# Performance work log

Hardware: AMD Instinct MI355X
Metric: run time of the kernel (lower is better)

Reference implementation:

```python
import jax, jax.numpy as jnp
import numpy as np

B, C, IMG, P = 32, 3, 224, 16
HID, L, NH, DH, INTER, NCLS = 768, 12, 12, 64, 3072, 1000
GP = IMG // P  # 14 patches per side
S = GP * GP + 1  # 197 tokens
EPS = 1e-5  # torch LayerNorm default


def layer_norm(x, scale, bias):
    mu = jnp.mean(x, axis=-1, keepdims=True)
    var = jnp.mean(jnp.square(x - mu), axis=-1, keepdims=True)
    return (x - mu) * jax.lax.rsqrt(var + EPS) * scale + bias


def setup_inputs() -> dict:
    key = jax.random.key(0)
    ks = jax.random.split(key, 16)
    s = 0.02
    d = {
        "x": jax.random.normal(ks[0], (B, C, IMG, IMG), jnp.float32),
        "conv_w": jax.random.normal(ks[1], (HID, C, P, P), jnp.float32) * s,
        "conv_b": jnp.zeros((HID,), jnp.float32),
        "cls_token": jax.random.normal(ks[2], (1, 1, HID), jnp.float32),
        "pos_emb": jax.random.normal(ks[3], (1, S, HID), jnp.float32) * s,
        "ln1_s": jnp.ones((L, HID), jnp.float32),
        "ln1_b": jnp.zeros((L, HID), jnp.float32),
        "wq": jax.random.normal(ks[4], (L, NH, HID, DH), jnp.float32) * s,
        "bq": jnp.zeros((L, NH, DH), jnp.float32),
        "wk": jax.random.normal(ks[5], (L, NH, HID, DH), jnp.float32) * s,
        "bk": jnp.zeros((L, NH, DH), jnp.float32),
        "wv": jax.random.normal(ks[6], (L, NH, HID, DH), jnp.float32) * s,
        "bv": jnp.zeros((L, NH, DH), jnp.float32),
        "wo": jax.random.normal(ks[7], (L, HID, HID), jnp.float32) * s,
        "bo": jnp.zeros((L, HID), jnp.float32),
        "ln2_s": jnp.ones((L, HID), jnp.float32),
        "ln2_b": jnp.zeros((L, HID), jnp.float32),
        "w1": jax.random.normal(ks[8], (L, HID, INTER), jnp.float32) * s,
        "b1": jnp.zeros((L, INTER), jnp.float32),
        "w2": jax.random.normal(ks[9], (L, INTER, HID), jnp.float32) * s,
        "b2": jnp.zeros((L, HID), jnp.float32),
        "head_w": jax.random.normal(ks[10], (HID, NCLS), jnp.float32) * s,
        "head_b": jnp.zeros((NCLS,), jnp.float32),
    }
    return d


def vit_forward(x, conv_w, conv_b, cls_token, pos_emb, ln1_s, ln1_b,
                wq, bq, wk, bk, wv, bv, wo, bo, ln2_s, ln2_b,
                w1, b1, w2, b2, head_w, head_b):
    # Patch embedding: conv stride=kernel=P  ==  patch extract + matmul
    xp = x.reshape(B, C, GP, P, GP, P)
    h = jnp.einsum('bcipjq,dcpq->bijd', xp, conv_w) + conv_b  # [B,GP,GP,HID]
    h = h.reshape(B, GP * GP, HID)
    h = jnp.concatenate([jnp.broadcast_to(cls_token, (B, 1, HID)), h], axis=1)
    h = h + pos_emb  # [B,S,HID]

    scale = 1.0 / np.sqrt(DH).astype(np.float32)
    for l in range(L):
        # --- multi-head attention (per-head linears expressed as stacked einsum) ---
        hn = layer_norm(h, ln1_s[l], ln1_b[l])
        q = jnp.einsum('bsd,hdk->bhsk', hn, wq[l]) + bq[l][None, :, None, :]
        k = jnp.einsum('bsd,hdk->bhsk', hn, wk[l]) + bk[l][None, :, None, :]
        v = jnp.einsum('bsd,hdk->bhsk', hn, wv[l]) + bv[l][None, :, None, :]
        scores = jnp.einsum('bhsk,bhtk->bhst', q, k) * scale
        probs = jax.nn.softmax(scores, axis=-1)
        att = jnp.einsum('bhst,bhtk->bhsk', probs, v)  # [B,NH,S,DH]
        att = att.transpose(0, 2, 1, 3).reshape(B, S, HID)  # concat heads on last dim
        h = h + att @ wo[l] + bo[l]
        # --- MLP ---
        hn = layer_norm(h, ln2_s[l], ln2_b[l])
        m = jax.nn.gelu(hn @ w1[l] + b1[l], approximate=False)
        h = h + m @ w2[l] + b2[l]

    # classifier on [CLS] token
    return h[:, 0, :] @ head_w + head_b  # [B, NCLS]


def reference(x, conv_w, conv_b, cls_token, pos_emb, ln1_s, ln1_b,
              wq, bq, wk, bk, wv, bv, wo, bo, ln2_s, ln2_b,
              w1, b1, w2, b2, head_w, head_b):
    return vit_forward(x, conv_w, conv_b, cls_token, pos_emb, ln1_s, ln1_b,
                       wq, bq, wk, bk, wv, bv, wo, bo, ln2_s, ln2_b,
                       w1, b1, w2, b2, head_w, head_b)
```

## Files before the change

### kernel.cpp

```cpp
#include <hip/hip_runtime.h>
#include <hip/hip_bf16.h>
#include <math.h>


using bf16 = __hip_bfloat16;
typedef __attribute__((ext_vector_type(8))) short short8;
typedef __attribute__((ext_vector_type(4))) float floatx4;

__device__ __forceinline__ void async_copy16(const bf16* g, bf16* l) {
    __builtin_amdgcn_global_load_lds(
        (const __attribute__((address_space(1))) void*)g,
        (__attribute__((address_space(3))) void*)l, 16, 0, 0);
}

__device__ __forceinline__ void wave_sync_vm0() {
    asm volatile("s_waitcnt vmcnt(0)" ::: "memory");
    __builtin_amdgcn_s_barrier();
    asm volatile("" ::: "memory");
}

template<int OUT_BF16, int ACT_GELU, int RESID>
__global__ __launch_bounds__(512, 4) void gemm_nt(
    const bf16* __restrict__ A, const bf16* __restrict__ B, void* __restrict__ Cout,
    const float* __restrict__ resid, const float* __restrict__ bias, float scale,
    int M, int N, int K, int lda, int ldb, int ldc,
    int batchInner, long sAi, long sAo, long sBi, long sBo, long sCi, long sCo)
{
    __shared__ __align__(16) bf16 As[2][128 * 32];
    __shared__ __align__(16) bf16 Bs[2][128 * 32];

    const int bz = blockIdx.z;
    const int bi = bz % batchInner, bo = bz / batchInner;
    const bf16* Ab = A + (long)bi * sAi + (long)bo * sAo;
    const bf16* Bb = B + (long)bi * sBi + (long)bo * sBo;
    const long coff = (long)bi * sCi + (long)bo * sCo;

    const int nbx = gridDim.x;
    const int nwg = nbx * gridDim.y;
    const int orig = blockIdx.y * nbx + blockIdx.x;
    const int q8 = nwg >> 3, r8 = nwg & 7;
    const int xcd = orig & 7, sidx = orig >> 3;
    const int wg = (xcd < r8 ? xcd * (q8 + 1) : r8 * (q8 + 1) + (xcd - r8) * q8) + sidx;
    const int m0 = (wg / nbx) << 7;
    const int n0 = (wg % nbx) << 7;

    const int tid  = threadIdx.x;
    const int lane = tid & 63;
    const int wave = tid >> 6;
    const int wrow = (wave >> 1) << 5;
    const int wcol = (wave & 1) << 6;
    const int quad = lane >> 4;
    const int l16  = lane & 15;

    floatx4 acc[2][4];
#pragma unroll
    for (int i = 0; i < 2; i++)
#pragma unroll
        for (int j = 0; j < 4; j++) acc[i][j] = (floatx4)0.0f;

    const int rIn = lane >> 2;
    const int seg = (lane & 3) << 3;
    const int rA = wave * 16 + rIn;
    const long aOff = (long)min(m0 + rA, M - 1) * lda + seg;
    const long bOff = (long)min(n0 + rA, N - 1) * ldb + seg;

    auto stage = [&](int buf, int kt) {
        const long kb = (long)kt << 5;
        async_copy16(Ab + aOff + kb, &As[buf][wave * 512]);
        async_copy16(Bb + bOff + kb, &Bs[buf][wave * 512]);
    };

    auto compute = [&](const bf16* __restrict__ Asb, const bf16* __restrict__ Bsb) {
        short8 af[2], bfr[4];
#pragma unroll
        for (int i = 0; i < 2; i++)
            af[i]  = *(const short8*)(&Asb[(wrow + i * 16 + l16) * 32 + quad * 8]);
#pragma unroll
        for (int j = 0; j < 4; j++)
            bfr[j] = *(const short8*)(&Bsb[(wcol + j * 16 + l16) * 32 + quad * 8]);
#pragma unroll
        for (int i = 0; i < 2; i++)
#pragma unroll
            for (int j = 0; j < 4; j++)
                acc[i][j] = __builtin_amdgcn_mfma_f32_16x16x32_bf16(
                    af[i], bfr[j], acc[i][j], 0, 0, 0);
    };

    const int kTiles = K >> 5;
    stage(0, 0);
    for (int kt = 0; kt < kTiles; kt += 2) {
        wave_sync_vm0();
        if (kt + 1 < kTiles) stage(1, kt + 1);
        compute(As[0], Bs[0]);
        if (kt + 1 < kTiles) {
            wave_sync_vm0();
            if (kt + 2 < kTiles) stage(0, kt + 2);
            compute(As[1], Bs[1]);
        }
    }

#pragma unroll
    for (int i = 0; i < 2; i++) {
        const int rbase = m0 + wrow + i * 16 + quad * 4;
#pragma unroll
        for (int j = 0; j < 4; j++) {
            const int col = n0 + wcol + j * 16 + l16;
            if (col >= N) continue;
            const float bval = bias ? bias[col] : 0.0f;
#pragma unroll
            for (int r = 0; r < 4; r++) {
                const int row = rbase + r;
                if (row >= M) continue;
                const long idx = coff + (long)row * ldc + col;
                float v = acc[i][j][r] * scale + bval;
                if (RESID)    v += resid[idx];
                if (ACT_GELU) v = 0.5f * v * (1.0f + erff(v * 0.70710678118654752f));
                if (OUT_BF16) ((bf16*)Cout)[idx] = __float2bfloat16(v);
                else          ((float*)Cout)[idx] = v;
            }
        }
    }
}

__global__ __launch_bounds__(256) void transpose_cvt(
    const float* __restrict__ src, bf16* __restrict__ dst, int K, int N,
    int srcLd, int dstLd, int batchInner, long sSi, long sSo, long sDi, long sDo)
{
    __shared__ float t[32][33];
    const int bz = blockIdx.z;
    const int bi = bz % batchInner, bo = bz / batchInner;
    const float* S = src + (long)bi * sSi + (long)bo * sSo;
    bf16* D = dst + (long)bi * sDi + (long)bo * sDo;
    const int k0 = blockIdx.y << 5, n0 = blockIdx.x << 5;
    const int tx = threadIdx.x & 31, ty = threadIdx.x >> 5;
#pragma unroll
    for (int i = 0; i < 32; i += 8) {
        int k = k0 + ty + i, n = n0 + tx;
        if (k < K && n < N) t[ty + i][tx] = S[(long)k * srcLd + n];
    }
    __syncthreads();
#pragma unroll
    for (int i = 0; i < 32; i += 8) {
        int n = n0 + ty + i, k = k0 + tx;
        if (n < N && k < K) D[(long)n * dstLd + k] = __float2bfloat16(t[tx][ty + i]);
    }
}

__global__ void cvt_f2b(const float* __restrict__ s, bf16* __restrict__ d, int n) {
    int i = blockIdx.x * 256 + threadIdx.x;
    if (i < n) d[i] = __float2bfloat16(s[i]);
}

__global__ void pack_qkv_bias(const float* __restrict__ bq, const float* __restrict__ bk,
                              const float* __restrict__ bv, float* __restrict__ qb) {
    int i = blockIdx.x * 256 + threadIdx.x;
    int l = i / 2304, n = i % 2304;
    float v = (n < 768) ? bq[l * 768 + n]
            : (n < 1536) ? bk[l * 768 + n - 768]
                         : bv[l * 768 + n - 1536];
    qb[i] = v;
}

__global__ __launch_bounds__(256) void im2col_k(const float* __restrict__ x, bf16* __restrict__ out) {
    const int row = blockIdx.x;
    const int b = row / 196, r = row % 196, gi = r / 14, gj = r % 14;
    const float* xb = x + (long)b * 3 * 224 * 224;
    bf16* o = out + (long)row * 768;
    const int tid = threadIdx.x;
#pragma unroll
    for (int i = 0; i < 3; i++) {
        int col = tid + (i << 8);
        int c = col >> 8, rem = col & 255, p = rem >> 4, q = rem & 15;
        o[col] = __float2bfloat16(xb[((long)c * 224 + gi * 16 + p) * 224 + gj * 16 + q]);
    }
}

__global__ __launch_bounds__(256) void assemble_k(const float* __restrict__ hp,
                                                  const float* __restrict__ cls,
                                                  const float* __restrict__ pos,
                                                  float* __restrict__ h) {
    const int row = blockIdx.x;
    const int b = row / 197, t = row % 197;
    float* o = h + (long)row * 768;
    const float* p = pos + (long)t * 768;
    const int tid = threadIdx.x;
#pragma unroll
    for (int i = 0; i < 3; i++) {
        int c = tid + (i << 8);
        float v = (t == 0) ? cls[c] : hp[((long)(b * 196 + t - 1)) * 768 + c];
        o[c] = v + p[c];
    }
}

__global__ __launch_bounds__(256) void layernorm_k(const float* __restrict__ h,
                                                   const float* __restrict__ gamma,
                                                   const float* __restrict__ beta,
                                                   bf16* __restrict__ out) {
    const int row = blockIdx.x;
    const float* x = h + (long)row * 768;
    const int tid = threadIdx.x;
    float v[3], s = 0.f, ss = 0.f;
#pragma unroll
    for (int i = 0; i < 3; i++) { v[i] = x[tid + (i << 8)]; s += v[i]; ss += v[i] * v[i]; }
#pragma unroll
    for (int o = 32; o; o >>= 1) { s += __shfl_xor(s, o); ss += __shfl_xor(ss, o); }
    __shared__ float red[8];
    const int wave = tid >> 6, lane = tid & 63;
    if (lane == 0) { red[wave] = s; red[4 + wave] = ss; }
    __syncthreads();
    if (tid == 0) {
        red[0] = red[0] + red[1] + red[2] + red[3];
        red[4] = red[4] + red[5] + red[6] + red[7];
    }
    __syncthreads();
    const float mu  = red[0] * (1.0f / 768.0f);
    const float var = red[4] * (1.0f / 768.0f) - mu * mu;
    const float inv = rsqrtf(var + 1e-5f);
    bf16* o = out + (long)row * 768;
#pragma unroll
    for (int i = 0; i < 3; i++) {
        int c = tid + (i << 8);
        o[c] = __float2bfloat16((v[i] - mu) * inv * gamma[c] + beta[c]);
    }
}

__global__ __launch_bounds__(256) void transpose_v(const bf16* __restrict__ qkv,
                                                   bf16* __restrict__ vT) {
    __shared__ bf16 t[64][65];
    const int t0 = blockIdx.x << 6;
    const int bz = blockIdx.y;
    const int b = bz / 12, hh = bz % 12;
    const int tx = threadIdx.x & 63, ty = threadIdx.x >> 6;
#pragma unroll
    for (int i = 0; i < 64; i += 4) {
        int tt = t0 + ty + i;
        bf16 v = __float2bfloat16(0.0f);
        if (tt < 197) v = qkv[((long)(b * 197 + tt)) * 2304 + 1536 + hh * 64 + tx];
        t[ty + i][tx] = v;
    }
    __syncthreads();
    bf16* d = vT + (long)bz * 14336;
#pragma unroll
    for (int i = 0; i < 64; i += 4) {
        int tt = t0 + tx;
        if (tt < 224) d[(long)(ty + i) * 224 + tt] = t[tx][ty + i];
    }
}

__global__ __launch_bounds__(256) void softmax_k(bf16* __restrict__ sc) {
    const int row = blockIdx.x * 4 + (threadIdx.x >> 6);
    const int lane = threadIdx.x & 63;
    bf16* s = sc + (long)row * 224;
    float v0 = __bfloat162float(s[lane]);
    float v1 = __bfloat162float(s[64 + lane]);
    float v2 = __bfloat162float(s[128 + lane]);
    float v3 = (192 + lane < 197) ? __bfloat162float(s[192 + lane]) : -1e30f;
    float m = fmaxf(fmaxf(v0, v1), fmaxf(v2, v3));
#pragma unroll
    for (int o = 32; o; o >>= 1) m = fmaxf(m, __shfl_xor(m, o));
    float e0 = __expf(v0 - m), e1 = __expf(v1 - m), e2 = __expf(v2 - m);
    float e3 = (192 + lane < 197) ? __expf(v3 - m) : 0.0f;
    float t = e0 + e1 + e2 + e3;
#pragma unroll
    for (int o = 32; o; o >>= 1) t += __shfl_xor(t, o);
    const float inv = 1.0f / t;
    s[lane]        = __float2bfloat16(e0 * inv);
    s[64 + lane]   = __float2bfloat16(e1 * inv);
    s[128 + lane]  = __float2bfloat16(e2 * inv);
    if (192 + lane < 224) s[192 + lane] = __float2bfloat16(e3 * inv);
}

__global__ __launch_bounds__(256) void extract_cls(const float* __restrict__ h,
                                                   bf16* __restrict__ hcls) {
    const int b = blockIdx.x, tid = threadIdx.x;
#pragma unroll
    for (int i = 0; i < 3; i++) {
        int c = tid + (i << 8);
        hcls[(long)b * 768 + c] = __float2bfloat16(h[(long)b * 197 * 768 + c]);
    }
}

extern "C" void kernel_launch(void* const* d_in, const int* in_sizes, int n_in,
                              void* d_out, int out_size, void* d_ws, size_t ws_size,
                              hipStream_t stream)
{
    (void)in_sizes; (void)n_in; (void)out_size; (void)ws_size;
    const float* x      = (const float*)d_in[0];
    const float* conv_w = (const float*)d_in[1];
    const float* conv_b = (const float*)d_in[2];
    const float* cls    = (const float*)d_in[3];
    const float* pos    = (const float*)d_in[4];
    const float* ln1_s  = (const float*)d_in[5];
    const float* ln1_b  = (const float*)d_in[6];
    const float* wq     = (const float*)d_in[7];
    const float* bq     = (const float*)d_in[8];
    const float* wk     = (const float*)d_in[9];
    const float* bk     = (const float*)d_in[10];
    const float* wv     = (const float*)d_in[11];
    const float* bv     = (const float*)d_in[12];
    const float* wo     = (const float*)d_in[13];
    const float* bo     = (const float*)d_in[14];
    const float* ln2_s  = (const float*)d_in[15];
    const float* ln2_b  = (const float*)d_in[16];
    const float* w1     = (const float*)d_in[17];
    const float* b1     = (const float*)d_in[18];
    const float* w2     = (const float*)d_in[19];
    const float* b2     = (const float*)d_in[20];
    const float* head_w = (const float*)d_in[21];
    const float* head_b = (const float*)d_in[22];
    float* out = (float*)d_out;

    char* ws = (char*)d_ws;
    size_t off = 0;
    auto take = [&](size_t bytes) -> char* {
        char* p = ws + off; off += (bytes + 255) & ~(size_t)255; return p;
    };
    float* h    = (float*)take(6304UL * 768 * 4);
    bf16*  hn   = (bf16*) take(6304UL * 768 * 2);
    bf16*  qkv  = (bf16*) take(6304UL * 2304 * 2);
    bf16*  att  = (bf16*) take(6304UL * 768 * 2);
    bf16*  Wqkv = (bf16*) take(12UL * 2304 * 768 * 2);
    bf16*  Wo   = (bf16*) take(12UL * 768 * 768 * 2);
    bf16*  W1   = (bf16*) take(12UL * 768 * 3072 * 2);
    bf16*  W2   = (bf16*) take(12UL * 768 * 3072 * 2);
    bf16*  Wp   = (bf16*) take(589824UL * 2);
    bf16*  Wh   = (bf16*) take(768000UL * 2);
    float* qb   = (float*)take(27648UL * 4);
    bf16*  hcls = (bf16*) take(24576UL * 2);
    char*  scr  = take(46UL * 1024 * 1024);
    bf16*  scores = (bf16*)scr;
    bf16*  vT     = (bf16*)(scr + 384UL * 197 * 224 * 2);
    bf16*  inter  = (bf16*)scr;
    bf16*  Apatch = (bf16*)scr;
    float* hpatch = (float*)(scr + ((6272UL * 768 * 2 + 255) & ~(size_t)255));

    cvt_f2b<<<2304, 256, 0, stream>>>(conv_w, Wp, 589824);
    transpose_cvt<<<dim3(2, 24, 144), 256, 0, stream>>>(wq, Wqkv,           768, 64, 64, 768, 12, 49152, 589824, 49152, 1769472);
    transpose_cvt<<<dim3(2, 24, 144), 256, 0, stream>>>(wk, Wqkv + 589824,  768, 64, 64, 768, 12, 49152, 589824, 49152, 1769472);
    transpose_cvt<<<dim3(2, 24, 144), 256, 0, stream>>>(wv, Wqkv + 1179648, 768, 64, 64, 768, 12, 49152, 589824, 49152, 1769472);
    transpose_cvt<<<dim3(24, 24, 12), 256, 0, stream>>>(wo, Wo, 768, 768, 768, 768, 12, 589824, 0, 589824, 0);
    transpose_cvt<<<dim3(96, 24, 12), 256, 0, stream>>>(w1, W1, 768, 3072, 3072, 768, 12, 2359296, 0, 2359296, 0);
    transpose_cvt<<<dim3(24, 96, 12), 256, 0, stream>>>(w2, W2, 3072, 768, 768, 3072, 12, 2359296, 0, 2359296, 0);
    transpose_cvt<<<dim3(32, 24, 1), 256, 0, stream>>>(head_w, Wh, 768, 1000, 1000, 768, 1, 0, 0, 0, 0);
    pack_qkv_bias<<<108, 256, 0, stream>>>(bq, bk, bv, qb);

    im2col_k<<<6272, 256, 0, stream>>>(x, Apatch);
    gemm_nt<0, 0, 0><<<dim3(6, 49, 1), 512, 0, stream>>>(
        Apatch, Wp, hpatch, nullptr, conv_b, 1.0f,
        6272, 768, 768, 768, 768, 768, 1, 0, 0, 0, 0, 0, 0);
    assemble_k<<<6304, 256, 0, stream>>>(hpatch, cls, pos, h);

    for (int l = 0; l < 12; ++l) {
        layernorm_k<<<6304, 256, 0, stream>>>(h, ln1_s + l * 768, ln1_b + l * 768, hn);
        gemm_nt<1, 0, 0><<<dim3(18, 50, 1), 512, 0, stream>>>(
            hn, Wqkv + (size_t)l * 1769472, qkv, nullptr, qb + l * 2304, 1.0f,
            6304, 2304, 768, 768, 768, 2304, 1, 0, 0, 0, 0, 0, 0);
        transpose_v<<<dim3(4, 384), 256, 0, stream>>>(qkv, vT);
        gemm_nt<1, 0, 0><<<dim3(2, 2, 384), 512, 0, stream>>>(
            qkv, qkv + 768, scores, nullptr, nullptr, 0.125f,
            197, 197, 64, 2304, 2304, 224,
            12, 64, 197L * 2304, 64, 197L * 2304, 44128, 529536);
        softmax_k<<<18912, 256, 0, stream>>>(scores);
        gemm_nt<1, 0, 0><<<dim3(1, 2, 384), 512, 0, stream>>>(
            scores, vT, att, nullptr, nullptr, 1.0f,
            197, 64, 224, 224, 224, 768,
            12, 44128, 529536, 14336, 172032, 64, 151296);
        gemm_nt<0, 0, 1><<<dim3(6, 50, 1), 512, 0, stream>>>(
            att, Wo + (size_t)l * 589824, h, h, bo + l * 768, 1.0f,
            6304, 768, 768, 768, 768, 768, 1, 0, 0, 0, 0, 0, 0);
        layernorm_k<<<6304, 256, 0, stream>>>(h, ln2_s + l * 768, ln2_b + l * 768, hn);
        gemm_nt<1, 1, 0><<<dim3(24, 50, 1), 512, 0, stream>>>(
            hn, W1 + (size_t)l * 2359296, inter, nullptr, b1 + l * 3072, 1.0f,
            6304, 3072, 768, 768, 768, 3072, 1, 0, 0, 0, 0, 0, 0);
        gemm_nt<0, 0, 1><<<dim3(6, 50, 1), 512, 0, stream>>>(
            inter, W2 + (size_t)l * 2359296, h, h, b2 + l * 768, 1.0f,
            6304, 768, 3072, 3072, 3072, 768, 1, 0, 0, 0, 0, 0, 0);
    }

    extract_cls<<<32, 256, 0, stream>>>(h, hcls);
    gemm_nt<0, 0, 0><<<dim3(8, 1, 1), 512, 0, stream>>>(
        hcls, Wh, out, nullptr, head_b, 1.0f,
        32, 1000, 768, 768, 768, 1000, 1, 0, 0, 0, 0, 0, 0);
}
```

Before: 4.033 ms.

## Deepen GEMM LDS pipeline to four stages with partial vmcnt waits

Replaces the double-buffered GEMM main loop with a four-buffer ring that keeps three tiles of global-to-LDS loads in flight. Each iteration waits only for the oldest tile (vmcnt(4)) rather than draining every outstanding load, aiming to hide more global memory latency. In exchange, LDS use doubles to 64KB per block, which may lower occupancy against the launch bound of 4 blocks, and the vmcnt counts assume exactly two loads per thread per stage.

```diff
diff --git a/kernel.cpp b/kernel.cpp
--- a/kernel.cpp
+++ b/kernel.cpp
@@ -11,12 +11,6 @@
     __builtin_amdgcn_global_load_lds(
         (const __attribute__((address_space(1))) void*)g,
         (__attribute__((address_space(3))) void*)l, 16, 0, 0);
-}
-
-__device__ __forceinline__ void wave_sync_vm0() {
-    asm volatile("s_waitcnt vmcnt(0)" ::: "memory");
-    __builtin_amdgcn_s_barrier();
-    asm volatile("" ::: "memory");
 }
 
 template<int OUT_BF16, int ACT_GELU, int RESID>
@@ -26,8 +20,8 @@
     int M, int N, int K, int lda, int ldb, int ldc,
     int batchInner, long sAi, long sAo, long sBi, long sBo, long sCi, long sCo)
 {
-    __shared__ __align__(16) bf16 As[2][128 * 32];
-    __shared__ __align__(16) bf16 Bs[2][128 * 32];
+    __shared__ __align__(16) bf16 As[4][128 * 32];
+    __shared__ __align__(16) bf16 Bs[4][128 * 32];
 
     const int bz = blockIdx.z;
     const int bi = bz % batchInner, bo = bz / batchInner;
@@ -87,17 +81,33 @@
     };
 
     const int kTiles = K >> 5;
-    stage(0, 0);
-    for (int kt = 0; kt < kTiles; kt += 2) {
-        wave_sync_vm0();
-        if (kt + 1 < kTiles) stage(1, kt + 1);
-        compute(As[0], Bs[0]);
-        if (kt + 1 < kTiles) {
-            wave_sync_vm0();
-            if (kt + 2 < kTiles) stage(0, kt + 2);
-            compute(As[1], Bs[1]);
-        }
-    }
+    const int pre = kTiles < 3 ? kTiles : 3;
+    for (int t = 0; t < pre; ++t) stage(t, t);
+
+    int kt = 0;
+    for (; kt < kTiles - 3; ++kt) {
+        asm volatile("s_waitcnt vmcnt(4)" ::: "memory");
+        __builtin_amdgcn_s_barrier();
+        asm volatile("" ::: "memory");
+        stage((kt + 3) & 3, kt + 3);
+        compute(As[kt & 3], Bs[kt & 3]);
+    }
+    if (kTiles - kt >= 3) {
+        asm volatile("s_waitcnt vmcnt(4)" ::: "memory");
+        __builtin_amdgcn_s_barrier();
+        asm volatile("" ::: "memory");
+        compute(As[kt & 3], Bs[kt & 3]); ++kt;
+    }
+    if (kTiles - kt >= 2) {
+        asm volatile("s_waitcnt vmcnt(2)" ::: "memory");
+        __builtin_amdgcn_s_barrier();
+        asm volatile("" ::: "memory");
+        compute(As[kt & 3], Bs[kt & 3]); ++kt;
+    }
+    asm volatile("s_waitcnt vmcnt(0)" ::: "memory");
+    __builtin_amdgcn_s_barrier();
+    asm volatile("" ::: "memory");
+    compute(As[kt & 3], Bs[kt & 3]);
 
 #pragma unroll
     for (int i = 0; i < 2; i++) {
```

Result: slower. 4.227 ms (+4.8%).
